# Kernel optimization log

Measured on AMD Instinct MI355X. Metric: run time of the kernel, lower is better.

Reference implementation:

```python
import jax, jax.numpy as jnp
import numpy as np

E = 8        # n_experts
K = 2        # top_k
D = 1024     # n_embed
H = 2048     # moe_n_hidden
B, T = 4, 2048


def setup_inputs() -> dict:
    key = jax.random.key(0)
    ks = jax.random.split(key, 6)
    s = 0.02
    return {
        "x": jax.random.normal(ks[0], (B, T, D), dtype=jnp.float32),
        "Wr": jax.random.normal(ks[1], (D, E), dtype=jnp.float32) * s,   # router weight
        "W1": jax.random.normal(ks[2], (E, D, 2 * H), dtype=jnp.float32) * s,
        "b1": jnp.zeros((E, 2 * H), dtype=jnp.float32),
        "W2": jax.random.normal(ks[3], (E, H, D), dtype=jnp.float32) * s,
        "b2": jnp.zeros((E, D), dtype=jnp.float32),
    }


def reference(x, Wr, W1, b1, W2, b2):
    b, t, d = x.shape
    # router logits (noise=0, temp=1.0)
    z = jnp.einsum('btd,de->bte', x, Wr)                 # [B,T,E]
    vals, idx = jax.lax.top_k(z, K)                      # [B,T,K]
    gates = jax.nn.softmax(vals, axis=-1)                # [B,T,K]
    # combine weights per (token, expert): sum_k gate_k * 1[idx_k == e]
    onehot = jax.nn.one_hot(idx, E, dtype=x.dtype)       # [B,T,K,E]
    comb = jnp.einsum('btk,btke->bte', gates, onehot).reshape(b * t, E)
    xf = x.reshape(b * t, d)                             # [N,D]
    out = jnp.zeros_like(xf)
    for e in range(E):  # fixed small loop over structurally-distinct experts
        ab = xf @ W1[e] + b1[e]                          # [N,2H]
        a, bb = jnp.split(ab, 2, axis=-1)
        h = jax.nn.silu(a) * bb                          # swiGLU
        y = h @ W2[e] + b2[e]                            # [N,D]
        out = out + comb[:, e:e + 1] * y
    return out.reshape(b, t, d)
```

## Files before the change

kernel.cpp:

```cpp
#include <hip/hip_runtime.h>


#define N_TOK 8192
#define DIM   1024
#define HID   2048
#define NEXP  8
#define NK    (N_TOK * 2)
#define MAXT1 136
#define G1Y   272

typedef __attribute__((ext_vector_type(8))) short short8;
typedef __attribute__((ext_vector_type(4))) float f32x4;

#define BARX() __builtin_amdgcn_s_barrier()
#define FEN()  asm volatile("" ::: "memory")
#define VMW0() asm volatile("s_waitcnt vmcnt(0)" ::: "memory")
#define PRIO(p) __builtin_amdgcn_s_setprio(p)

static __device__ __forceinline__ unsigned short f2bf(float f) {
  unsigned int u = __float_as_uint(f);
  u += 0x7fffu + ((u >> 16) & 1u);
  return (unsigned short)(u >> 16);
}

static __device__ __forceinline__ void glds16(const void* g, void* l) {
  __builtin_amdgcn_global_load_lds(
      (const __attribute__((address_space(1))) unsigned int*)g,
      (__attribute__((address_space(3))) unsigned int*)l, 16, 0, 0);
}

__device__ __forceinline__ void transpose_tile(const float* __restrict__ s,
                                               unsigned short* __restrict__ d,
                                               int R, int C, int c0, int r0,
                                               unsigned short (*tT)[68]) {
  int tid = threadIdx.x;
  int c = tid & 63, rq = tid >> 6;
#pragma unroll
  for (int q = 0; q < 4; ++q) {
    int rb = q * 16 + rq * 4;
    ushort4 v;
    v.x = f2bf(s[(size_t)(r0 + rb + 0) * C + c0 + c]);
    v.y = f2bf(s[(size_t)(r0 + rb + 1) * C + c0 + c]);
    v.z = f2bf(s[(size_t)(r0 + rb + 2) * C + c0 + c]);
    v.w = f2bf(s[(size_t)(r0 + rb + 3) * C + c0 + c]);
    *(ushort4*)&tT[c][rb] = v;
  }
  __syncthreads();
#pragma unroll
  for (int it = 0; it < 4; ++it) {
    int idx = it * 256 + tid;
    int cc = idx >> 4;
    int r4 = (idx & 15) * 4;
    *(ushort4*)(d + (size_t)(c0 + cc) * R + r0 + r4) = *(const ushort4*)&tT[cc][r4];
  }
}

__global__ __launch_bounds__(256) void prep_k(
    const float* __restrict__ x, const float* __restrict__ Wr,
    const float* __restrict__ W1,
    unsigned short* __restrict__ w1t,
    unsigned short* __restrict__ xb, int* __restrict__ te,
    float* __restrict__ tg) {
  __shared__ unsigned short tT[64][68];
  int bid = blockIdx.x;
  if (bid < 8192) {
    int z = bid >> 10, rem = bid & 1023;
    int c0 = (rem & 63) * 64, r0 = (rem >> 6) * 64;
    transpose_tile(W1 + (size_t)z * DIM * 2 * HID,
                   w1t + (size_t)z * DIM * 2 * HID, DIM, 2 * HID, c0, r0, tT);
  } else {
    int n = (bid - 8192) * 4 + (threadIdx.x >> 6);
    int lane = threadIdx.x & 63;
    float z[8];
#pragma unroll
    for (int e = 0; e < 8; ++e) z[e] = 0.f;
    const float* xr = x + (size_t)n * DIM;
    unsigned short* xbr = xb + (size_t)n * DIM;
#pragma unroll 4
    for (int i = 0; i < DIM / 64; ++i) {
      int d = lane + i * 64;
      float xv = xr[d];
      xbr[d] = f2bf(xv);
      float4 w0 = *(const float4*)(Wr + (size_t)d * 8);
      float4 w1 = *(const float4*)(Wr + (size_t)d * 8 + 4);
      z[0] += xv * w0.x; z[1] += xv * w0.y; z[2] += xv * w0.z; z[3] += xv * w0.w;
      z[4] += xv * w1.x; z[5] += xv * w1.y; z[6] += xv * w1.z; z[7] += xv * w1.w;
    }
    for (int off = 32; off; off >>= 1)
#pragma unroll
      for (int e = 0; e < 8; ++e) z[e] += __shfl_down(z[e], off);
    if (lane == 0) {
      int e0 = 0; float v0 = z[0];
#pragma unroll
      for (int e = 1; e < 8; ++e) if (z[e] > v0) { v0 = z[e]; e0 = e; }
      int e1 = -1; float v1 = -3.4e38f;
#pragma unroll
      for (int e = 0; e < 8; ++e) if (e != e0 && z[e] > v1) { v1 = z[e]; e1 = e; }
      float r = expf(v1 - v0);
      float s0 = 1.f / (1.f + r);
      te[n * 2] = e0; te[n * 2 + 1] = e1;
      tg[n * 2] = s0; tg[n * 2 + 1] = r * s0;
    }
  }
}

__global__ __launch_bounds__(1024) void sortscan_k(
    const int* __restrict__ te, const float* __restrict__ tg,
    int* __restrict__ offs, int* __restrict__ tl128,
    int* __restrict__ rows, float* __restrict__ rowg) {
  __shared__ int hist[8];
  __shared__ int curs[8];
  int tid = threadIdx.x;
  if (tid < 8) hist[tid] = 0;
  __syncthreads();
  for (int i = tid; i < NK; i += 1024) atomicAdd(&hist[te[i]], 1);
  __syncthreads();
  if (tid == 0) {
    int o = 0, t1 = 0;
    offs[0] = 0; tl128[0] = 0;
    for (int e = 0; e < NEXP; ++e) {
      curs[e] = o;
      o += hist[e];
      offs[e + 1] = o;
      t1 += (hist[e] + 127) >> 7;
      tl128[e + 1] = t1;
    }
  }
  __syncthreads();
  for (int i = tid; i < NK; i += 1024) {
    int e = te[i];
    int pos = atomicAdd(&curs[e], 1);
    rows[pos] = i >> 1;
    rowg[pos] = tg[i];
  }
}

template <int GID>
__global__ __launch_bounds__(256, 3) void moe_gemm2p(
    const unsigned short* __restrict__ Asrc,
    const unsigned short* __restrict__ Wt,
    const float* __restrict__ bias,
    unsigned short* __restrict__ hb,
    float* __restrict__ out,
    const int* __restrict__ rows,
    const float* __restrict__ rowg,
    const int* __restrict__ offs,
    const int* __restrict__ tl,
    const float* __restrict__ W2f,
    unsigned short* __restrict__ w2td,
    float* __restrict__ outz) {
  constexpr int KD = (GID == 0) ? DIM : HID;
  constexpr int NT = KD / 32;
  __shared__ unsigned short smem[16384];

  int bt = blockIdx.y;
  if (GID == 0 && bt >= MAXT1) {
    if (bt < MAXT1 + 128) {
      int t = (bt - MAXT1) * 32 + (int)blockIdx.x;
      int z = t >> 9, rem = t & 511;
      int c0 = (rem & 15) * 64, r0 = (rem >> 4) * 64;
      transpose_tile(W2f + (size_t)z * HID * DIM,
                     w2td + (size_t)z * HID * DIM, HID, DIM, c0, r0,
                     (unsigned short(*)[68])smem);
    } else {
      int t = (bt - MAXT1 - 128) * 32 + (int)blockIdx.x;
      float4* o4 = (float4*)outz;
      int idx = t * 256 + threadIdx.x;
#pragma unroll
      for (int i = 0; i < 32; ++i) o4[idx + i * 65536] = (float4){0.f, 0.f, 0.f, 0.f};
    }
    return;
  }
  if (bt >= tl[NEXP]) return;
  int e = 0;
  while (e < NEXP - 1 && bt >= tl[e + 1]) ++e;
  int rt = bt - tl[e];
  int base = offs[e];
  int cntE = offs[e + 1] - base;
  int row0 = rt * 128;
  int jb = blockIdx.x;

  int tid = threadIdx.x, lane = tid & 63, w = tid >> 6;
  int wr = w >> 1, wc = w & 1;

  int g8 = (((lane & 3) ^ ((lane >> 3) & 3)) * 8);
  const unsigned short* aP[2];
  const unsigned short* bP[2];
  int aD[2], bD[2];
#pragma unroll
  for (int s = 0; s < 2; ++s) {
    int rA = w * 16 + (lane >> 2) + s * 64;
    int rr = row0 + rA; rr = rr < cntE ? rr : cntE - 1;
    if (GID == 0) {
      int tok = rows[base + rr];
      aP[s] = Asrc + (size_t)tok * DIM + g8;
    } else {
      aP[s] = Asrc + (size_t)(base + rr) * HID + g8;
    }
    aD[s] = (w * 16 + s * 64) * 32;
    int rB = w * 16 + (lane >> 2) + s * 64;
    if (GID == 0) {
      int j0 = jb * 64;
      int u = rB & 63, wcb = rB >> 6;
      int hcol = j0 + wcb * 32 + (u & 31);
      int w1row = hcol + (u >> 5) * HID;
      bP[s] = Wt + ((size_t)e * 2 * HID + w1row) * DIM + g8;
    } else {
      bP[s] = Wt + ((size_t)e * DIM + (jb * 128 + rB)) * HID + g8;
    }
    bD[s] = (w * 16 + s * 64) * 32;
  }

  auto stg = [&](int t, int nxt) {
    if (t < NT) {
      glds16(aP[0] + (size_t)t * 32, smem + nxt * 4096 + aD[0]);
      glds16(aP[1] + (size_t)t * 32, smem + nxt * 4096 + aD[1]);
      glds16(bP[0] + (size_t)t * 32, smem + 8192 + nxt * 4096 + bD[0]);
      glds16(bP[1] + (size_t)t * 32, smem + 8192 + nxt * 4096 + bD[1]);
    }
  };

  int kg = lane >> 4, coll = lane & 15;
  int koff = ((kg ^ ((lane >> 1) & 3)) * 8);
  unsigned aoff[4], boff[4];
#pragma unroll
  for (int m = 0; m < 4; ++m) aoff[m] = (unsigned)((wr * 64 + m * 16 + coll) * 32 + koff);
#pragma unroll
  for (int n = 0; n < 4; ++n) boff[n] = (unsigned)((wc * 64 + n * 16 + coll) * 32 + koff);

  f32x4 acc[4][4];
#pragma unroll
  for (int m = 0; m < 4; ++m)
#pragma unroll
    for (int n = 0; n < 4; ++n) acc[m][n] = (f32x4){0.f, 0.f, 0.f, 0.f};

  short8 a[4], b[4];

  stg(0, 0);
  VMW0(); FEN(); BARX(); FEN();

  int cur = 0;
  for (int t = 0; t < NT; ++t) {
    stg(t + 1, cur ^ 1);
#pragma unroll
    for (int m = 0; m < 4; ++m)
      a[m] = *(const short8*)(smem + cur * 4096 + aoff[m]);
#pragma unroll
    for (int n = 0; n < 4; ++n)
      b[n] = *(const short8*)(smem + 8192 + cur * 4096 + boff[n]);
    PRIO(1);
#pragma unroll
    for (int m = 0; m < 4; ++m)
#pragma unroll
      for (int n = 0; n < 4; ++n)
        acc[m][n] = __builtin_amdgcn_mfma_f32_16x16x32_bf16(a[m], b[n], acc[m][n], 0, 0, 0);
    PRIO(0);
    VMW0(); FEN(); BARX(); FEN();
    cur ^= 1;
  }

  int rowl = lane >> 4;
  if (GID == 0) {
    int j0 = jb * 64;
#pragma unroll
    for (int n = 0; n < 2; ++n) {
      int hcol = j0 + wc * 32 + n * 16 + coll;
      float ba = bias[e * 2 * HID + hcol];
      float bb = bias[e * 2 * HID + HID + hcol];
#pragma unroll
      for (int m = 0; m < 4; ++m)
#pragma unroll
        for (int j = 0; j < 4; ++j) {
          int grow = row0 + wr * 64 + m * 16 + rowl * 4 + j;
          if (grow < cntE) {
            float av = acc[m][n][j] + ba;
            float bv = acc[m][n + 2][j] + bb;
            float hv = av / (1.f + __expf(-av)) * bv;
            hb[(size_t)(base + grow) * HID + hcol] = f2bf(hv);
          }
        }
    }
  } else {
#pragma unroll
    for (int m = 0; m < 4; ++m)
#pragma unroll
      for (int j = 0; j < 4; ++j) {
        int grow = row0 + wr * 64 + m * 16 + rowl * 4 + j;
        if (grow < cntE) {
          int tok = rows[base + grow];
          float g = rowg[base + grow];
#pragma unroll
          for (int n = 0; n < 4; ++n) {
            int col = jb * 128 + wc * 64 + n * 16 + coll;
            atomicAdd(&out[(size_t)tok * DIM + col],
                      g * (acc[m][n][j] + bias[e * DIM + col]));
          }
        }
      }
  }
}

extern "C" void kernel_launch(void* const* d_in, const int* in_sizes, int n_in,
                              void* d_out, int out_size, void* d_ws, size_t ws_size,
                              hipStream_t stream) {
  (void)in_sizes; (void)n_in; (void)out_size;
  const float* x  = (const float*)d_in[0];
  const float* Wr = (const float*)d_in[1];
  const float* W1 = (const float*)d_in[2];
  const float* b1 = (const float*)d_in[3];
  const float* W2 = (const float*)d_in[4];
  const float* b2 = (const float*)d_in[5];
  float* out = (float*)d_out;
  char* ws = (char*)d_ws;

  const size_t o_xb   = 0;
  const size_t o_w1t  = o_xb   + (size_t)N_TOK * DIM * 2;
  const size_t o_w2t  = o_w1t  + (size_t)NEXP * 2 * HID * DIM * 2;
  const size_t o_hb   = o_w2t  + (size_t)NEXP * DIM * HID * 2;
  const size_t o_rows = o_hb   + (size_t)NK * HID * 2;
  const size_t o_rowg = o_rows + (size_t)NK * 4;
  const size_t o_te   = o_rowg + (size_t)NK * 4;
  const size_t o_tg   = o_te   + (size_t)NK * 4;
  const size_t o_offs = o_tg   + (size_t)NK * 4;
  const size_t o_t1   = o_offs + 64;
  const size_t need   = o_t1   + 64;
  if (ws_size < need) return;

  unsigned short* xb  = (unsigned short*)(ws + o_xb);
  unsigned short* w1t = (unsigned short*)(ws + o_w1t);
  unsigned short* w2t = (unsigned short*)(ws + o_w2t);
  unsigned short* hb  = (unsigned short*)(ws + o_hb);
  int*   rows = (int*)(ws + o_rows);
  float* rowg = (float*)(ws + o_rowg);
  int*   te   = (int*)(ws + o_te);
  float* tg   = (float*)(ws + o_tg);
  int*   offs = (int*)(ws + o_offs);
  int*   tl128 = (int*)(ws + o_t1);

  prep_k<<<10240, 256, 0, stream>>>(x, Wr, W1, w1t, xb, te, tg);
  sortscan_k<<<1, 1024, 0, stream>>>(te, tg, offs, tl128, rows, rowg);
  moe_gemm2p<0><<<dim3(HID / 64, G1Y), 256, 0, stream>>>(
      xb, w1t, b1, hb, nullptr, rows, rowg, offs, tl128, W2, w2t, out);
  moe_gemm2p<1><<<dim3(DIM / 128, MAXT1), 256, 0, stream>>>(
      hb, w2t, b2, nullptr, out, rows, rowg, offs, tl128, nullptr, nullptr, nullptr);
}
```

Measured before the change: 418.6 us.

## Triple-buffer the GEMM shared-memory pipeline with partial vmcnt waits

Moves the MoE GEMM main loop from double to triple buffering of LDS tiles. Two stages are prefetched, each iteration waits only for the older stage (vmcnt(4)), then issues the load for t+2, and there is one barrier per iteration instead of a full drain after compute. This is meant to hide global-to-LDS load latency behind MFMA work. The cost is more LDS per block (48KB vs 32KB), which may reduce occupancy, and it also relies on the barrier ordering to avoid overwriting a buffer that is still being read.

```diff
diff --git a/kernel.cpp b/kernel.cpp
--- a/kernel.cpp
+++ b/kernel.cpp
@@ -14,6 +14,7 @@
 
 #define BARX() __builtin_amdgcn_s_barrier()
 #define FEN()  asm volatile("" ::: "memory")
+#define VMW4() asm volatile("s_waitcnt vmcnt(4)" ::: "memory")
 #define VMW0() asm volatile("s_waitcnt vmcnt(0)" ::: "memory")
 #define PRIO(p) __builtin_amdgcn_s_setprio(p)
 
@@ -136,7 +137,7 @@
 }
 
 template <int GID>
-__global__ __launch_bounds__(256, 3) void moe_gemm2p(
+__global__ __launch_bounds__(256, 3) void moe_gemm3b(
     const unsigned short* __restrict__ Asrc,
     const unsigned short* __restrict__ Wt,
     const float* __restrict__ bias,
@@ -151,7 +152,7 @@
     float* __restrict__ outz) {
   constexpr int KD = (GID == 0) ? DIM : HID;
   constexpr int NT = KD / 32;
-  __shared__ unsigned short smem[16384];
+  __shared__ unsigned short smem[24576];
 
   int bt = blockIdx.y;
   if (GID == 0 && bt >= MAXT1) {
@@ -211,12 +212,12 @@
     bD[s] = (w * 16 + s * 64) * 32;
   }
 
-  auto stg = [&](int t, int nxt) {
+  auto stg = [&](int t, int buf) {
     if (t < NT) {
-      glds16(aP[0] + (size_t)t * 32, smem + nxt * 4096 + aD[0]);
-      glds16(aP[1] + (size_t)t * 32, smem + nxt * 4096 + aD[1]);
-      glds16(bP[0] + (size_t)t * 32, smem + 8192 + nxt * 4096 + bD[0]);
-      glds16(bP[1] + (size_t)t * 32, smem + 8192 + nxt * 4096 + bD[1]);
+      glds16(aP[0] + (size_t)t * 32, smem + buf * 4096 + aD[0]);
+      glds16(aP[1] + (size_t)t * 32, smem + buf * 4096 + aD[1]);
+      glds16(bP[0] + (size_t)t * 32, smem + 12288 + buf * 4096 + bD[0]);
+      glds16(bP[1] + (size_t)t * 32, smem + 12288 + buf * 4096 + bD[1]);
     }
   };
 
@@ -237,17 +238,20 @@
   short8 a[4], b[4];
 
   stg(0, 0);
-  VMW0(); FEN(); BARX(); FEN();
-
-  int cur = 0;
+  stg(1, 1);
+
+  int rb = 0;
   for (int t = 0; t < NT; ++t) {
-    stg(t + 1, cur ^ 1);
+    if (t == NT - 1) { VMW0(); } else { VMW4(); }
+    FEN(); BARX(); FEN();
+    int wb = rb + 2; if (wb >= 3) wb -= 3;
+    stg(t + 2, wb);
 #pragma unroll
     for (int m = 0; m < 4; ++m)
-      a[m] = *(const short8*)(smem + cur * 4096 + aoff[m]);
+      a[m] = *(const short8*)(smem + rb * 4096 + aoff[m]);
 #pragma unroll
     for (int n = 0; n < 4; ++n)
-      b[n] = *(const short8*)(smem + 8192 + cur * 4096 + boff[n]);
+      b[n] = *(const short8*)(smem + 12288 + rb * 4096 + boff[n]);
     PRIO(1);
 #pragma unroll
     for (int m = 0; m < 4; ++m)
@@ -255,8 +259,7 @@
       for (int n = 0; n < 4; ++n)
         acc[m][n] = __builtin_amdgcn_mfma_f32_16x16x32_bf16(a[m], b[n], acc[m][n], 0, 0, 0);
     PRIO(0);
-    VMW0(); FEN(); BARX(); FEN();
-    cur ^= 1;
+    rb = (rb + 1 == 3) ? 0 : rb + 1;
   }
 
   int rowl = lane >> 4;
@@ -339,8 +342,8 @@
 
   prep_k<<<10240, 256, 0, stream>>>(x, Wr, W1, w1t, xb, te, tg);
   sortscan_k<<<1, 1024, 0, stream>>>(te, tg, offs, tl128, rows, rowg);
-  moe_gemm2p<0><<<dim3(HID / 64, G1Y), 256, 0, stream>>>(
+  moe_gemm3b<0><<<dim3(HID / 64, G1Y), 256, 0, stream>>>(
       xb, w1t, b1, hb, nullptr, rows, rowg, offs, tl128, W2, w2t, out);
-  moe_gemm2p<1><<<dim3(DIM / 128, MAXT1), 256, 0, stream>>>(
+  moe_gemm3b<1><<<dim3(DIM / 128, MAXT1), 256, 0, stream>>>(
       hb, w2t, b2, nullptr, out, rows, rowg, offs, tl128, nullptr, nullptr, nullptr);
 }
```

Result: faster. 403.1 us (-3.7%).
